# Kernel optimization log

Measured on AMD Instinct MI355X. Metric: run time of the kernel, lower is better.

Reference implementation:

```python
import jax, jax.numpy as jnp
import numpy as np

EPS = 1e-5      # eps used in abs() and log()
BN_EPS = 1e-5   # torch BatchNorm2d default eps


def setup_inputs() -> dict:
    key = jax.random.key(0)
    ks = jax.random.split(key, 5)
    N, C, F, T = 16, 4, 257, 1000
    B, K = 8, 80
    xr = jax.random.normal(ks[0], (N, C, F, T), dtype=jnp.float32)
    xi = jax.random.normal(ks[1], (N, C, F, T), dtype=jnp.float32)
    # per-bin complex beamforming weights: (F, B, C) == Conv1d weight (B*F, 1, C) regrouped
    wr = jax.random.normal(ks[2], (F, B, C), dtype=jnp.float32) * 0.25
    wi = jax.random.normal(ks[3], (F, B, C), dtype=jnp.float32) * 0.25
    # nn.Linear(num_bins, spectra_filters, bias=False) weight: (K, F)
    w_proj = jax.random.normal(ks[4], (K, F), dtype=jnp.float32) * (1.0 / np.sqrt(F))
    gamma = jnp.ones((B,), dtype=jnp.float32)
    beta = jnp.zeros((B,), dtype=jnp.float32)
    return {"xr": xr, "xi": xi, "wr": wr, "wi": wi, "w_proj": w_proj,
            "gamma": gamma, "beta": beta}


def reference(xr, xi, wr, wi, w_proj, gamma, beta):
    # Grouped complex conv1d == per-bin complex beamform across mics:
    # out[n,b,t,f] = sum_c w[f,b,c] * x[n,c,f,t] (complex product)
    br = jnp.einsum('ncft,fbc->nbtf', xr, wr) - jnp.einsum('ncft,fbc->nbtf', xi, wi)
    bi = jnp.einsum('ncft,fbc->nbtf', xi, wr) + jnp.einsum('ncft,fbc->nbtf', xr, wi)
    mag = jnp.sqrt(br * br + bi * bi + EPS)              # (N, B, T, F)
    # Linear(F -> K), ReLU, log
    f = jax.nn.relu(jnp.einsum('nbtf,kf->nbtk', mag, w_proj))
    f = jnp.log(f + EPS)                                  # (N, B, T, K)
    # BatchNorm2d over channel axis B (training-mode batch statistics)
    mean = jnp.mean(f, axis=(0, 2, 3), keepdims=True)
    var = jnp.var(f, axis=(0, 2, 3), keepdims=True)
    f = (f - mean) * jax.lax.rsqrt(var + BN_EPS)
    f = f * gamma[None, :, None, None] + beta[None, :, None, None]
    N, B, T, K = f.shape
    # (N, B, T, K) -> (N, T, B*K)
    return jnp.transpose(f, (0, 2, 1, 3)).reshape(N, T, B * K)
```

## Files before the change

### kernel.cpp

```cpp
#include <hip/hip_runtime.h>
#include <math.h>

#define N_ 16
#define C_ 4
#define F_ 257
#define T_ 1000
#define B_ 8
#define K_ 80
#define BK_ 640
#define TT_ 16
#define NT_ 63
#define NBLK (N_ * NT_)
#define MSTR 262
#define WKS  80

#define WT_OFF   0
#define PART_OFF (128 * 1024)
#define SS_OFF   (PART_OFF + NBLK * 16 * 8)

__global__ __launch_bounds__(80) void k_wt(const float* __restrict__ wp,
                                           float* __restrict__ wT) {
    int f = blockIdx.x;
    int k = threadIdx.x;
    wT[f * WKS + k] = wp[k * F_ + f];
}

__global__ __launch_bounds__(256, 2) void k_fused(
    const float* __restrict__ xr, const float* __restrict__ xi,
    const float* __restrict__ wr, const float* __restrict__ wi,
    const float* __restrict__ wT,
    float* __restrict__ out, double* __restrict__ partials) {

    const int tid = threadIdx.x;
    const int bid = blockIdx.x;
    const int tt = bid % NT_;
    const int n  = bid / NT_;
    const int t0 = tt * TT_;

    __shared__ float magS[2][TT_][MSTR];
    __shared__ double redS1[4][4][2];
    __shared__ double redS2[4][4][2];

    const int t_loc = tid & 15;
    const int bq    = (tid >> 4) & 3;
    const int kg    = __builtin_amdgcn_readfirstlane(tid >> 6);

    const int sfr = tid >> 3;
    const int st2 = tid & 7;
    const int tb  = t0 + st2 * 2;
    const bool tload = (tb + 2 <= T_);

    float acc[2][20];
#pragma unroll
    for (int i = 0; i < 2; ++i)
#pragma unroll
        for (int j = 0; j < 20; ++j) acc[i][j] = 0.f;

    const float* xrn = xr + (size_t)n * C_ * F_ * T_;
    const float* xin = xi + (size_t)n * C_ * F_ * T_;

    float2 pxr[C_], pxi[C_];
    if (tload) {
        const float* xrp = xrn + (size_t)sfr * T_ + tb;
        const float* xip = xin + (size_t)sfr * T_ + tb;
#pragma unroll
        for (int c = 0; c < C_; ++c) {
            pxr[c] = *(const float2*)(xrp + (size_t)c * F_ * T_);
            pxi[c] = *(const float2*)(xip + (size_t)c * F_ * T_);
        }
    }

    for (int ch = 0; ch < 8; ++ch) {
        const int f0 = ch * 32;
        const int f  = f0 + sfr;
        const int pb = ch & 1;

        {
            float m[2][B_];
            if (tload) {
                float xrv[C_][2], xiv[C_][2];
#pragma unroll
                for (int c = 0; c < C_; ++c) {
                    xrv[c][0] = pxr[c].x; xrv[c][1] = pxr[c].y;
                    xiv[c][0] = pxi[c].x; xiv[c][1] = pxi[c].y;
                }
                const float* wrp = wr + (size_t)f * B_ * C_;
                const float* wip = wi + (size_t)f * B_ * C_;
#pragma unroll
                for (int b = 0; b < B_; ++b) {
                    float4 wrv = *(const float4*)(wrp + b * C_);
                    float4 wiv = *(const float4*)(wip + b * C_);
                    float wrc[4] = {wrv.x, wrv.y, wrv.z, wrv.w};
                    float wic[4] = {wiv.x, wiv.y, wiv.z, wiv.w};
#pragma unroll
                    for (int i = 0; i < 2; ++i) {
                        float br = 0.f, bi2 = 0.f;
#pragma unroll
                        for (int c = 0; c < C_; ++c) {
                            br  += xrv[c][i] * wrc[c] - xiv[c][i] * wic[c];
                            bi2 += xiv[c][i] * wrc[c] + xrv[c][i] * wic[c];
                        }
                        m[i][b] = sqrtf(br * br + bi2 * bi2 + 1e-5f);
                    }
                }
            } else {
#pragma unroll
                for (int i = 0; i < 2; ++i)
#pragma unroll
                    for (int b = 0; b < B_; ++b) m[i][b] = 0.f;
            }
#pragma unroll
            for (int i = 0; i < 2; ++i) {
                *(float4*)&magS[pb][st2 * 2 + i][sfr * 8] =
                    make_float4(m[i][0], m[i][1], m[i][2], m[i][3]);
                *(float4*)&magS[pb][st2 * 2 + i][sfr * 8 + 4] =
                    make_float4(m[i][4], m[i][5], m[i][6], m[i][7]);
            }
        }

        if (ch < 7 && tload) {
            const float* xrp = xrn + (size_t)(f0 + 32 + sfr) * T_ + tb;
            const float* xip = xin + (size_t)(f0 + 32 + sfr) * T_ + tb;
#pragma unroll
            for (int c = 0; c < C_; ++c) {
                pxr[c] = *(const float2*)(xrp + (size_t)c * F_ * T_);
                pxi[c] = *(const float2*)(xip + (size_t)c * F_ * T_);
            }
        }

        __syncthreads();

        const float* wchunk = wT + (size_t)f0 * WKS + kg * 20;
#pragma unroll 4
        for (int fc = 0; fc < 32; ++fc) {
            float2 mv = *(const float2*)&magS[pb][t_loc][fc * 8 + bq * 2];
            float wv[20];
#pragma unroll
            for (int j = 0; j < 20; ++j) wv[j] = wchunk[fc * WKS + j];
#pragma unroll
            for (int j = 0; j < 20; ++j) {
                acc[0][j] += mv.x * wv[j];
                acc[1][j] += mv.y * wv[j];
            }
        }
    }

    if (tid < 128) {
        int trow = tid >> 3;
        int b = tid & 7;
        int t = t0 + trow;
        float v = 0.f;
        if (t < T_) {
            const float* wrp = wr + (size_t)(256 * B_ + b) * C_;
            const float* wip = wi + (size_t)(256 * B_ + b) * C_;
            float br = 0.f, bi2 = 0.f;
#pragma unroll
            for (int c = 0; c < C_; ++c) {
                float xrv = xrn[((size_t)c * F_ + 256) * T_ + t];
                float xiv = xin[((size_t)c * F_ + 256) * T_ + t];
                br  += xrv * wrp[c] - xiv * wip[c];
                bi2 += xiv * wrp[c] + xrv * wip[c];
            }
            v = sqrtf(br * br + bi2 * bi2 + 1e-5f);
        }
        magS[0][trow][b] = v;
    }
    __syncthreads();
    {
        float2 mv = *(const float2*)&magS[0][t_loc][bq * 2];
        const float* wtail = wT + (size_t)256 * WKS + kg * 20;
#pragma unroll
        for (int j = 0; j < 20; ++j) {
            float wv = wtail[j];
            acc[0][j] += mv.x * wv;
            acc[1][j] += mv.y * wv;
        }
    }

    float s1f[2], s2f[2];
    s1f[0] = s1f[1] = s2f[0] = s2f[1] = 0.f;
    const int t = t0 + t_loc;
    if (t < T_) {
        float* obase = out + ((size_t)n * T_ + t) * BK_ + (bq * 2) * K_ + kg * 20;
#pragma unroll
        for (int i = 0; i < 2; ++i) {
            float vv[20];
#pragma unroll
            for (int j = 0; j < 20; ++j) {
                float v = fmaxf(acc[i][j], 0.0f);
                v = __logf(v + 1e-5f);
                vv[j] = v;
                s1f[i] += v;
                s2f[i] += v * v;
            }
            float* orow = obase + i * K_;
#pragma unroll
            for (int q = 0; q < 5; ++q)
                *(float4*)(orow + q * 4) =
                    make_float4(vv[q * 4], vv[q * 4 + 1], vv[q * 4 + 2], vv[q * 4 + 3]);
        }
    }
    const int wav = tid >> 6;
#pragma unroll
    for (int i = 0; i < 2; ++i) {
        double d1 = (double)s1f[i], d2 = (double)s2f[i];
#pragma unroll
        for (int off = 1; off < 16; off <<= 1) {
            d1 += __shfl_xor(d1, off);
            d2 += __shfl_xor(d2, off);
        }
        if (t_loc == 0) { redS1[wav][bq][i] = d1; redS2[wav][bq][i] = d2; }
    }
    __syncthreads();
    if (tid < 8) {
        int bqi = tid >> 1, ii = tid & 1;
        partials[(size_t)bid * 16 + tid] =
            redS1[0][bqi][ii] + redS1[1][bqi][ii] + redS1[2][bqi][ii] + redS1[3][bqi][ii];
    } else if (tid >= 64 && tid < 72) {
        int id = tid - 64;
        int bqi = id >> 1, ii = id & 1;
        partials[(size_t)bid * 16 + 8 + id] =
            redS2[0][bqi][ii] + redS2[1][bqi][ii] + redS2[2][bqi][ii] + redS2[3][bqi][ii];
    }
}

__global__ __launch_bounds__(256) void k_bnstats(
    const double* __restrict__ partials,
    const float* __restrict__ gamma, const float* __restrict__ beta,
    float* __restrict__ ss) {
    const int b = threadIdx.x >> 5;
    const int i = threadIdx.x & 31;
    double s1 = 0.0, s2 = 0.0;
    for (int j = i; j < NBLK; j += 32) {
        s1 += partials[(size_t)j * 16 + b];
        s2 += partials[(size_t)j * 16 + 8 + b];
    }
#pragma unroll
    for (int off = 16; off; off >>= 1) {
        s1 += __shfl_down(s1, off);
        s2 += __shfl_down(s2, off);
    }
    if (i == 0) {
        const double cnt = (double)N_ * T_ * K_;
        double mean = s1 / cnt;
        double var = s2 / cnt - mean * mean;
        float scale = gamma[b] * (float)(1.0 / sqrt(var + 1e-5));
        float shift = beta[b] - (float)mean * scale;
        ss[b] = scale;
        ss[B_ + b] = shift;
    }
}

__global__ __launch_bounds__(256) void k_bnapply(float* __restrict__ out,
                                                 const float* __restrict__ ss) {
    size_t i4 = (size_t)blockIdx.x * 256 + threadIdx.x;
    int k4 = (int)(i4 % (BK_ / 4));
    int b = k4 / (K_ / 4);
    float scale = ss[b], shift = ss[B_ + b];
    float4* p = (float4*)out + i4;
    float4 v = *p;
    v.x = v.x * scale + shift;
    v.y = v.y * scale + shift;
    v.z = v.z * scale + shift;
    v.w = v.w * scale + shift;
    *p = v;
}

extern "C" void kernel_launch(void* const* d_in, const int* in_sizes, int n_in,
                              void* d_out, int out_size, void* d_ws, size_t ws_size,
                              hipStream_t stream) {
    const float* xr = (const float*)d_in[0];
    const float* xi = (const float*)d_in[1];
    const float* wr = (const float*)d_in[2];
    const float* wi = (const float*)d_in[3];
    const float* w_proj = (const float*)d_in[4];
    const float* gamma = (const float*)d_in[5];
    const float* beta = (const float*)d_in[6];
    float* out = (float*)d_out;

    float* wT = (float*)((char*)d_ws + WT_OFF);
    double* partials = (double*)((char*)d_ws + PART_OFF);
    float* ss = (float*)((char*)d_ws + SS_OFF);

    k_wt<<<F_, 80, 0, stream>>>(w_proj, wT);
    k_fused<<<NBLK, 256, 0, stream>>>(xr, xi, wr, wi, wT, out, partials);
    k_bnstats<<<1, 256, 0, stream>>>(partials, gamma, beta, ss);
    k_bnapply<<<10000, 256, 0, stream>>>(out, ss);
}
```

Before: 159.8 us.

## Compute F-to-K projection with split-fp16 MFMA instead of scalar FP32 FMAs

The 256-bin projection GEMM moves from per-thread scalar FMAs onto MFMA 16x16x16 f16 instructions. Both the magnitudes and the projection weights are split into three fp16 pieces so the products keep near-FP32 accuracy, at the cost of six MFMAs per tile. Blocks grow to 512 threads, with one thread per (f, t) for the beamform stage and one wave per beam channel. The split weights are staged through LDS each chunk. Splitting adds conversion work and LDS traffic, and the output is now written as scalar stores instead of float4.

```diff
diff --git a/kernel.cpp b/kernel.cpp
--- a/kernel.cpp
+++ b/kernel.cpp
@@ -11,24 +11,56 @@
 #define TT_ 16
 #define NT_ 63
 #define NBLK (N_ * NT_)
-#define MSTR 262
-#define WKS  80
-
-#define WT_OFF   0
-#define PART_OFF (128 * 1024)
-#define SS_OFF   (PART_OFF + NBLK * 16 * 8)
+#define MSTR 264
+
+typedef _Float16 half4 __attribute__((ext_vector_type(4)));
+typedef _Float16 half8 __attribute__((ext_vector_type(8)));
+typedef float f32x4 __attribute__((ext_vector_type(4)));
+
+#define WSCALE   256.0f
+#define WUNSCALE 0.00390625f
+
+#define WP0_OFF   0
+#define WP1_OFF   (64 * 1024)
+#define WP2_OFF   (128 * 1024)
+#define WTAIL_OFF (192 * 1024)
+#define PART_OFF  (256 * 1024)
+#define SS_OFF    (PART_OFF + NBLK * 16 * 8)
 
 __global__ __launch_bounds__(80) void k_wt(const float* __restrict__ wp,
-                                           float* __restrict__ wT) {
-    int f = blockIdx.x;
-    int k = threadIdx.x;
-    wT[f * WKS + k] = wp[k * F_ + f];
-}
-
-__global__ __launch_bounds__(256, 2) void k_fused(
+                                           _Float16* __restrict__ wp0,
+                                           _Float16* __restrict__ wp1,
+                                           _Float16* __restrict__ wp2,
+                                           float* __restrict__ wtail) {
+    int blk = blockIdx.x;
+    int tid = threadIdx.x;
+    if (blk < 80) {
+        if (tid < 64) {
+            int ch = blk / 10, r = blk % 10, kt = r >> 1, ksub = r & 1;
+            int k = kt * 16 + (tid & 15);
+            int fb = ch * 32 + ksub * 16 + 4 * (tid >> 4);
+#pragma unroll
+            for (int j = 0; j < 4; ++j) {
+                float w = wp[k * F_ + fb + j] * WSCALE;
+                _Float16 w0 = (_Float16)w;
+                float r1 = (w - (float)w0) * 2048.0f;
+                _Float16 w1 = (_Float16)r1;
+                float r2 = (r1 - (float)w1) * 2048.0f;
+                _Float16 w2 = (_Float16)r2;
+                size_t o = ((size_t)blk * 64 + tid) * 4 + j;
+                wp0[o] = w0; wp1[o] = w1; wp2[o] = w2;
+            }
+        }
+    } else {
+        wtail[tid] = wp[tid * F_ + 256];
+    }
+}
+
+__global__ __launch_bounds__(512, 4) void k_fused(
     const float* __restrict__ xr, const float* __restrict__ xi,
     const float* __restrict__ wr, const float* __restrict__ wi,
-    const float* __restrict__ wT,
+    const _Float16* __restrict__ wp0, const _Float16* __restrict__ wp1,
+    const _Float16* __restrict__ wp2, const float* __restrict__ wtail,
     float* __restrict__ out, double* __restrict__ partials) {
 
     const int tid = threadIdx.x;
@@ -37,36 +69,38 @@
     const int n  = bid / NT_;
     const int t0 = tt * TT_;
 
-    __shared__ float magS[2][TT_][MSTR];
-    __shared__ double redS1[4][4][2];
-    __shared__ double redS2[4][4][2];
-
-    const int t_loc = tid & 15;
-    const int bq    = (tid >> 4) & 3;
-    const int kg    = __builtin_amdgcn_readfirstlane(tid >> 6);
-
-    const int sfr = tid >> 3;
-    const int st2 = tid & 7;
-    const int tb  = t0 + st2 * 2;
-    const bool tload = (tb + 2 <= T_);
-
-    float acc[2][20];
-#pragma unroll
-    for (int i = 0; i < 2; ++i)
-#pragma unroll
-        for (int j = 0; j < 20; ++j) acc[i][j] = 0.f;
+    __shared__ __attribute__((aligned(16))) float magS[2][TT_][MSTR];
+    __shared__ __attribute__((aligned(16))) _Float16 wfS[2][3][2560];
+    __shared__ float wtS[80];
+    __shared__ float magT[TT_][B_];
+
+    const int lane = tid & 63;
+    const int wv   = tid >> 6;
+
+    const int sfr = tid >> 4;
+    const int t_s = tid & 15;
+    const int tg  = t0 + t_s;
+    const bool tld = (tg < T_);
+
+    f32x4 accM[5], acc1[5], acc2[5];
+#pragma unroll
+    for (int kt = 0; kt < 5; ++kt) {
+        accM[kt] = (f32x4)0.0f;
+        acc1[kt] = (f32x4)0.0f;
+        acc2[kt] = (f32x4)0.0f;
+    }
 
     const float* xrn = xr + (size_t)n * C_ * F_ * T_;
     const float* xin = xi + (size_t)n * C_ * F_ * T_;
 
-    float2 pxr[C_], pxi[C_];
-    if (tload) {
-        const float* xrp = xrn + (size_t)sfr * T_ + tb;
-        const float* xip = xin + (size_t)sfr * T_ + tb;
+    if (tid < 80) wtS[tid] = wtail[tid];
+
+    float pxr[C_], pxi[C_];
+    if (tld) {
 #pragma unroll
         for (int c = 0; c < C_; ++c) {
-            pxr[c] = *(const float2*)(xrp + (size_t)c * F_ * T_);
-            pxi[c] = *(const float2*)(xip + (size_t)c * F_ * T_);
+            pxr[c] = xrn[((size_t)c * F_ + sfr) * T_ + tg];
+            pxi[c] = xin[((size_t)c * F_ + sfr) * T_ + tg];
         }
     }
 
@@ -75,72 +109,80 @@
         const int f  = f0 + sfr;
         const int pb = ch & 1;
 
+#pragma unroll
+        for (int r = 0; r < 2; ++r) {
+            int idx = tid + r * 512;
+            if (idx < 960) {
+                int term = idx / 320;
+                int u = idx - term * 320;
+                const _Float16* src =
+                    (term == 0 ? wp0 : (term == 1 ? wp1 : wp2)) + ch * 2560 + u * 8;
+                *(half8*)&wfS[pb][term][u * 8] = *(const half8*)src;
+            }
+        }
+
         {
-            float m[2][B_];
-            if (tload) {
-                float xrv[C_][2], xiv[C_][2];
-#pragma unroll
-                for (int c = 0; c < C_; ++c) {
-                    xrv[c][0] = pxr[c].x; xrv[c][1] = pxr[c].y;
-                    xiv[c][0] = pxi[c].x; xiv[c][1] = pxi[c].y;
-                }
+            float m[B_];
+            if (tld) {
                 const float* wrp = wr + (size_t)f * B_ * C_;
                 const float* wip = wi + (size_t)f * B_ * C_;
 #pragma unroll
                 for (int b = 0; b < B_; ++b) {
                     float4 wrv = *(const float4*)(wrp + b * C_);
                     float4 wiv = *(const float4*)(wip + b * C_);
-                    float wrc[4] = {wrv.x, wrv.y, wrv.z, wrv.w};
-                    float wic[4] = {wiv.x, wiv.y, wiv.z, wiv.w};
-#pragma unroll
-                    for (int i = 0; i < 2; ++i) {
-                        float br = 0.f, bi2 = 0.f;
-#pragma unroll
-                        for (int c = 0; c < C_; ++c) {
-                            br  += xrv[c][i] * wrc[c] - xiv[c][i] * wic[c];
-                            bi2 += xiv[c][i] * wrc[c] + xrv[c][i] * wic[c];
-                        }
-                        m[i][b] = sqrtf(br * br + bi2 * bi2 + 1e-5f);
-                    }
+                    float br  = pxr[0] * wrv.x + pxr[1] * wrv.y + pxr[2] * wrv.z + pxr[3] * wrv.w
+                              - pxi[0] * wiv.x - pxi[1] * wiv.y - pxi[2] * wiv.z - pxi[3] * wiv.w;
+                    float bi2 = pxi[0] * wrv.x + pxi[1] * wrv.y + pxi[2] * wrv.z + pxi[3] * wrv.w
+                              + pxr[0] * wiv.x + pxr[1] * wiv.y + pxr[2] * wiv.z + pxr[3] * wiv.w;
+                    m[b] = sqrtf(br * br + bi2 * bi2 + 1e-5f);
                 }
             } else {
 #pragma unroll
-                for (int i = 0; i < 2; ++i)
-#pragma unroll
-                    for (int b = 0; b < B_; ++b) m[i][b] = 0.f;
-            }
-#pragma unroll
-            for (int i = 0; i < 2; ++i) {
-                *(float4*)&magS[pb][st2 * 2 + i][sfr * 8] =
-                    make_float4(m[i][0], m[i][1], m[i][2], m[i][3]);
-                *(float4*)&magS[pb][st2 * 2 + i][sfr * 8 + 4] =
-                    make_float4(m[i][4], m[i][5], m[i][6], m[i][7]);
-            }
-        }
-
-        if (ch < 7 && tload) {
-            const float* xrp = xrn + (size_t)(f0 + 32 + sfr) * T_ + tb;
-            const float* xip = xin + (size_t)(f0 + 32 + sfr) * T_ + tb;
+                for (int b = 0; b < B_; ++b) m[b] = 0.f;
+            }
+            *(float4*)&magS[pb][t_s][sfr * 8] = make_float4(m[0], m[1], m[2], m[3]);
+            *(float4*)&magS[pb][t_s][sfr * 8 + 4] = make_float4(m[4], m[5], m[6], m[7]);
+        }
+
+        if (ch < 7 && tld) {
+            const int f2 = f0 + 32 + sfr;
 #pragma unroll
             for (int c = 0; c < C_; ++c) {
-                pxr[c] = *(const float2*)(xrp + (size_t)c * F_ * T_);
-                pxi[c] = *(const float2*)(xip + (size_t)c * F_ * T_);
+                pxr[c] = xrn[((size_t)c * F_ + f2) * T_ + tg];
+                pxi[c] = xin[((size_t)c * F_ + f2) * T_ + tg];
             }
         }
 
         __syncthreads();
 
-        const float* wchunk = wT + (size_t)f0 * WKS + kg * 20;
-#pragma unroll 4
-        for (int fc = 0; fc < 32; ++fc) {
-            float2 mv = *(const float2*)&magS[pb][t_loc][fc * 8 + bq * 2];
-            float wv[20];
-#pragma unroll
-            for (int j = 0; j < 20; ++j) wv[j] = wchunk[fc * WKS + j];
-#pragma unroll
-            for (int j = 0; j < 20; ++j) {
-                acc[0][j] += mv.x * wv[j];
-                acc[1][j] += mv.y * wv[j];
+        {
+            const int tA = lane & 15;
+            const int g  = lane >> 4;
+#pragma unroll
+            for (int ks = 0; ks < 2; ++ks) {
+                half4 a0, a1, a2;
+#pragma unroll
+                for (int j = 0; j < 4; ++j) {
+                    float v = magS[pb][tA][(ks * 16 + 4 * g + j) * 8 + wv];
+                    _Float16 h0 = (_Float16)v;
+                    float r1 = (v - (float)h0) * 2048.0f;
+                    _Float16 h1 = (_Float16)r1;
+                    float r2 = (r1 - (float)h1) * 2048.0f;
+                    a0[j] = h0; a1[j] = h1; a2[j] = (_Float16)r2;
+                }
+#pragma unroll
+                for (int kt = 0; kt < 5; ++kt) {
+                    int fi = ((kt * 2 + ks) * 64 + lane) * 4;
+                    half4 b0 = *(const half4*)&wfS[pb][0][fi];
+                    half4 b1 = *(const half4*)&wfS[pb][1][fi];
+                    half4 b2 = *(const half4*)&wfS[pb][2][fi];
+                    accM[kt] = __builtin_amdgcn_mfma_f32_16x16x16f16(a0, b0, accM[kt], 0, 0, 0);
+                    acc1[kt] = __builtin_amdgcn_mfma_f32_16x16x16f16(a0, b1, acc1[kt], 0, 0, 0);
+                    acc1[kt] = __builtin_amdgcn_mfma_f32_16x16x16f16(a1, b0, acc1[kt], 0, 0, 0);
+                    acc2[kt] = __builtin_amdgcn_mfma_f32_16x16x16f16(a0, b2, acc2[kt], 0, 0, 0);
+                    acc2[kt] = __builtin_amdgcn_mfma_f32_16x16x16f16(a1, b1, acc2[kt], 0, 0, 0);
+                    acc2[kt] = __builtin_amdgcn_mfma_f32_16x16x16f16(a2, b0, acc2[kt], 0, 0, 0);
+                }
             }
         }
     }
@@ -163,64 +205,40 @@
             }
             v = sqrtf(br * br + bi2 * bi2 + 1e-5f);
         }
-        magS[0][trow][b] = v;
+        magT[trow][b] = v;
     }
     __syncthreads();
-    {
-        float2 mv = *(const float2*)&magS[0][t_loc][bq * 2];
-        const float* wtail = wT + (size_t)256 * WKS + kg * 20;
-#pragma unroll
-        for (int j = 0; j < 20; ++j) {
-            float wv = wtail[j];
-            acc[0][j] += mv.x * wv;
-            acc[1][j] += mv.y * wv;
-        }
-    }
-
-    float s1f[2], s2f[2];
-    s1f[0] = s1f[1] = s2f[0] = s2f[1] = 0.f;
-    const int t = t0 + t_loc;
-    if (t < T_) {
-        float* obase = out + ((size_t)n * T_ + t) * BK_ + (bq * 2) * K_ + kg * 20;
-#pragma unroll
-        for (int i = 0; i < 2; ++i) {
-            float vv[20];
-#pragma unroll
-            for (int j = 0; j < 20; ++j) {
-                float v = fmaxf(acc[i][j], 0.0f);
+
+    const int col = lane & 15;
+    const int g   = lane >> 4;
+    float s1 = 0.f, s2 = 0.f;
+#pragma unroll
+    for (int kt = 0; kt < 5; ++kt) {
+        f32x4 r = (accM[kt] + 4.8828125e-4f * acc1[kt]
+                   + 2.384185791015625e-7f * acc2[kt]) * WUNSCALE;
+#pragma unroll
+        for (int reg = 0; reg < 4; ++reg) {
+            int trow = 4 * g + reg;
+            int t = t0 + trow;
+            float sum = r[reg] + magT[trow][wv] * wtS[kt * 16 + col];
+            if (t < T_) {
+                float v = fmaxf(sum, 0.0f);
                 v = __logf(v + 1e-5f);
-                vv[j] = v;
-                s1f[i] += v;
-                s2f[i] += v * v;
-            }
-            float* orow = obase + i * K_;
-#pragma unroll
-            for (int q = 0; q < 5; ++q)
-                *(float4*)(orow + q * 4) =
-                    make_float4(vv[q * 4], vv[q * 4 + 1], vv[q * 4 + 2], vv[q * 4 + 3]);
-        }
-    }
-    const int wav = tid >> 6;
-#pragma unroll
-    for (int i = 0; i < 2; ++i) {
-        double d1 = (double)s1f[i], d2 = (double)s2f[i];
-#pragma unroll
-        for (int off = 1; off < 16; off <<= 1) {
-            d1 += __shfl_xor(d1, off);
-            d2 += __shfl_xor(d2, off);
-        }
-        if (t_loc == 0) { redS1[wav][bq][i] = d1; redS2[wav][bq][i] = d2; }
-    }
-    __syncthreads();
-    if (tid < 8) {
-        int bqi = tid >> 1, ii = tid & 1;
-        partials[(size_t)bid * 16 + tid] =
-            redS1[0][bqi][ii] + redS1[1][bqi][ii] + redS1[2][bqi][ii] + redS1[3][bqi][ii];
-    } else if (tid >= 64 && tid < 72) {
-        int id = tid - 64;
-        int bqi = id >> 1, ii = id & 1;
-        partials[(size_t)bid * 16 + 8 + id] =
-            redS2[0][bqi][ii] + redS2[1][bqi][ii] + redS2[2][bqi][ii] + redS2[3][bqi][ii];
+                out[((size_t)n * T_ + t) * BK_ + wv * K_ + kt * 16 + col] = v;
+                s1 += v;
+                s2 += v * v;
+            }
+        }
+    }
+    double d1 = (double)s1, d2 = (double)s2;
+#pragma unroll
+    for (int off = 32; off; off >>= 1) {
+        d1 += __shfl_xor(d1, off);
+        d2 += __shfl_xor(d2, off);
+    }
+    if (lane == 0) {
+        partials[(size_t)bid * 16 + wv] = d1;
+        partials[(size_t)bid * 16 + 8 + wv] = d2;
     }
 }
 
@@ -278,12 +296,15 @@
     const float* beta = (const float*)d_in[6];
     float* out = (float*)d_out;
 
-    float* wT = (float*)((char*)d_ws + WT_OFF);
+    _Float16* wp0 = (_Float16*)((char*)d_ws + WP0_OFF);
+    _Float16* wp1 = (_Float16*)((char*)d_ws + WP1_OFF);
+    _Float16* wp2 = (_Float16*)((char*)d_ws + WP2_OFF);
+    float* wtail = (float*)((char*)d_ws + WTAIL_OFF);
     double* partials = (double*)((char*)d_ws + PART_OFF);
     float* ss = (float*)((char*)d_ws + SS_OFF);
 
-    k_wt<<<F_, 80, 0, stream>>>(w_proj, wT);
-    k_fused<<<NBLK, 256, 0, stream>>>(xr, xi, wr, wi, wT, out, partials);
+    k_wt<<<81, 80, 0, stream>>>(w_proj, wp0, wp1, wp2, wtail);
+    k_fused<<<NBLK, 512, 0, stream>>>(xr, xi, wr, wi, wp0, wp1, wp2, wtail, out, partials);
     k_bnstats<<<1, 256, 0, stream>>>(partials, gamma, beta, ss);
     k_bnapply<<<10000, 256, 0, stream>>>(out, ss);
 }
```

Result: slower. 260.7 us (+63.1%).
